# Kernel tuning notes

Hardware: AMD Instinct MI355X
Metric: run time of the kernel (lower is better)

The kernel has to match this reference:

```python
import jax, jax.numpy as jnp
import numpy as np

B, N, DEG = 16, 2048, 16          # graphs, nodes per graph, avg out-degree
C_IN, HID, K = 64, 128, 32        # in_channels, hidden_channels, out_channels (clusters)
NT = B * N                        # total nodes
E = NT * DEG                      # total edges
GN_EPS = 1e-5


def setup_inputs() -> dict:
    key = jax.random.key(0)
    ks = jax.random.split(key, 6)
    x = jax.random.normal(ks[0], (NT, C_IN), jnp.float32)
    # within-graph random edges (sorted batch => node i belongs to graph i // N)
    src_l = jax.random.randint(ks[1], (E,), 0, N)
    dst_l = jax.random.randint(ks[2], (E,), 0, N)
    gid = jnp.repeat(jnp.arange(B, dtype=jnp.int32), N * DEG)
    edge_index = jnp.stack([gid * N + src_l, gid * N + dst_l]).astype(jnp.int32)
    batch = jnp.repeat(jnp.arange(B, dtype=jnp.int32), N)
    return dict(
        x=x, edge_index=edge_index, batch=batch,
        gn_weight=jnp.ones((C_IN,), jnp.float32),
        gn_bias=jnp.zeros((C_IN,), jnp.float32),
        gn_mean_scale=jnp.ones((C_IN,), jnp.float32),
        w1=jax.random.normal(ks[3], (C_IN, HID), jnp.float32) / np.float32(np.sqrt(C_IN)),
        b1=jnp.zeros((HID,), jnp.float32),
        w2=jax.random.normal(ks[4], (HID, K), jnp.float32) / np.float32(np.sqrt(HID)),
        b2=jnp.zeros((K,), jnp.float32),
    )


def reference(x, gn_weight, gn_bias, gn_mean_scale, w1, b1, w2, b2, edge_index, batch):
    # ---- GraphNorm (per-graph mean/var with learnable mean scale) ----
    ones_n = jnp.ones((NT,), x.dtype)
    cnt = jax.ops.segment_sum(ones_n, batch, num_segments=B)[:, None]        # [B,1]
    mean = jax.ops.segment_sum(x, batch, num_segments=B) / cnt              # [B,C]
    xm = x - gn_mean_scale * mean[batch]
    var = jax.ops.segment_sum(xm * xm, batch, num_segments=B) / cnt         # [B,C]
    h = gn_weight * xm / jnp.sqrt(var + GN_EPS)[batch] + gn_bias            # [NT,C_IN]

    # ---- GCNConv (add self-loops, symmetric D^-1/2 (A+I) D^-1/2) ----
    src, dst = edge_index[0], edge_index[1]
    loop = jnp.arange(NT, dtype=src.dtype)
    src_l = jnp.concatenate([src, loop])
    dst_l = jnp.concatenate([dst, loop])
    deg = jax.ops.segment_sum(jnp.ones_like(src_l, x.dtype), dst_l, num_segments=NT)
    dinv = jnp.where(deg > 0, jax.lax.rsqrt(deg), 0.0)
    norm = dinv[src_l] * dinv[dst_l]                                        # [E+NT]
    hw = h @ w1                                                             # [NT,HID]
    h = jax.ops.segment_sum(norm[:, None] * hw[src_l], dst_l, num_segments=NT) + b1
    h = jax.nn.selu(h)

    # ---- to_dense_batch / to_dense_adj (uniform graph sizes -> mask all True) ----
    xd = h.reshape(B, N, HID)                                               # [B,N,F]
    adj = jnp.zeros((B, N, N), x.dtype).at[batch[src], src % N, dst % N].add(1.0)

    # ---- DMoNPooling ----
    s = jax.nn.softmax(xd @ w2 + b2, axis=-1)                               # [B,N,K]
    out = jax.nn.selu(jnp.einsum('bnk,bnf->bkf', s, xd))                    # [B,K,F]
    sta = jnp.einsum('bnk,bnm->bkm', s, adj)                                # [B,K,N]
    out_adj = jnp.einsum('bkm,bml->bkl', sta, s)                            # [B,K,K]

    degrees = adj.sum(-1)                                                   # [B,N]
    m = degrees.sum(-1) / 2                                                 # [B]
    ca = jnp.einsum('bnk,bn->bk', s, degrees)                               # [B,K]
    normalizer = ca[:, :, None] * ca[:, None, :] / 2 / m[:, None, None]
    spectral_loss = (-jnp.einsum('bkk->b', out_adj - normalizer) / (2 * m)).mean()

    ss = jnp.einsum('bnk,bnl->bkl', s, s)                                   # [B,K,K]
    ss_fro = jnp.sqrt(jnp.sum(ss * ss, axis=(-2, -1), keepdims=True))
    eye = jnp.eye(K, dtype=x.dtype)
    diff = ss / ss_fro - eye / jnp.sqrt(jnp.float32(K))
    ortho_loss = jnp.sqrt(jnp.sum(diff * diff, axis=(-2, -1))).mean()

    cluster_size = s.sum(1)                                                 # [B,K]
    cluster_loss = (jnp.linalg.norm(cluster_size, axis=1) / N
                    * jnp.sqrt(jnp.float32(K)) - 1).mean()
    # (coarsened-adj renormalization in DMoNPooling is unused by Net's outputs)

    return jax.nn.log_softmax(out, axis=-1), spectral_loss + ortho_loss + cluster_loss, s
```

## Files before the change

### kernel.cpp

```cpp
#include <hip/hip_runtime.h>
#include <cmath>

static constexpr int B_  = 16;
static constexpr int N_  = 2048;
static constexpr int NT_ = 32768;
static constexpr int E_  = 524288;

static constexpr size_t OFF_HSC    = 0;
static constexpr size_t OFF_XD     = 2097152;
static constexpr size_t OFF_SWS    = 6291456;
static constexpr size_t OFF_PART   = 7340032;
static constexpr size_t OFF_DINV   = 9437184;
static constexpr size_t OFF_GSP    = 9469952;
static constexpr size_t OFF_GSP2   = 9478144;
static constexpr size_t OFF_SSP    = 9486336;
static constexpr size_t OFF_CAP    = 10010624;
static constexpr size_t OFF_CSP    = 10027008;
static constexpr size_t OFF_SPECP  = 10043392;
static constexpr size_t OFF_ICNTO  = 10043904;
static constexpr size_t OFF_IROWS  = 10076672;
static constexpr size_t OFF_IESRC  = 10109444;

__device__ __forceinline__ float selu_f(float x) {
  return 1.0507009873554805f * (x > 0.f ? x : 1.6732632423543772f * expm1f(x));
}

__device__ __forceinline__ float block_sum_bcast(float v, float* sm) {
  int lane = threadIdx.x & 63, w = threadIdx.x >> 6;
#pragma unroll
  for (int off = 32; off; off >>= 1) v += __shfl_down(v, off);
  __syncthreads();
  if (lane == 0) sm[w] = v;
  __syncthreads();
  return sm[0] + sm[1] + sm[2] + sm[3];
}

__global__ __launch_bounds__(1024) void k_graph(const int* ei, const float* x,
                                                int* rows, int* esrc, int* cout_,
                                                float* dinv, float* gsp, float* gsp2) {
  __shared__ int hin[2048], hout[2048], sb[1024];
  __shared__ float l1[16][64], l2[16][64];
  int blk = blockIdx.x;
  int tid = threadIdx.x;
  if (blk < 16) {
    int g = blk;
    int nbase = g * 2048;
    int ebase = g * 32768;
    hin[tid] = 0; hin[tid + 1024] = 0;
    hout[tid] = 0; hout[tid + 1024] = 0;
    __syncthreads();
    for (int i = tid; i < 32768; i += 1024) {
      int s = ei[ebase + i];
      int d = ei[E_ + ebase + i];
      atomicAdd(&hout[s - nbase], 1);
      atomicAdd(&hin[d - nbase], 1);
    }
    __syncthreads();
    int a = hin[2 * tid], b2 = hin[2 * tid + 1];
    sb[tid] = a + b2;
    __syncthreads();
    for (int off = 1; off < 1024; off <<= 1) {
      int add = (tid >= off) ? sb[tid - off] : 0;
      __syncthreads();
      sb[tid] += add;
      __syncthreads();
    }
    int pref = (tid > 0) ? sb[tid - 1] : 0;
    int r0 = ebase + pref, r1 = r0 + a;
    int n0 = nbase + 2 * tid;
    rows[n0] = r0; rows[n0 + 1] = r1;
    dinv[n0] = rsqrtf((float)(a + 1));
    dinv[n0 + 1] = rsqrtf((float)(b2 + 1));
    cout_[n0] = hout[2 * tid];
    cout_[n0 + 1] = hout[2 * tid + 1];
    if (blk == 15 && tid == 1023) rows[NT_] = E_;
    __syncthreads();
    hin[2 * tid] = r0; hin[2 * tid + 1] = r1;
    __syncthreads();
    for (int i = tid; i < 32768; i += 1024) {
      int s = ei[ebase + i];
      int d = ei[E_ + ebase + i];
      int pos = atomicAdd(&hin[d - nbase], 1);
      esrc[pos] = s;
    }
  } else {
    int gi = blk - 16;
    int b = gi >> 3, chunk = gi & 7;
    int c = tid & 63, r = tid >> 6;
    float s = 0.f, s2 = 0.f;
    const float* xb = x + ((size_t)b * N_ + (size_t)chunk * 256) * 64;
    for (int n = r; n < 256; n += 16) {
      float v = xb[n * 64 + c];
      s += v; s2 += v * v;
    }
    l1[r][c] = s; l2[r][c] = s2;
    __syncthreads();
    if (r == 0) {
      float t1 = 0.f, t2 = 0.f;
#pragma unroll
      for (int i = 0; i < 16; i++) { t1 += l1[i][c]; t2 += l2[i][c]; }
      gsp[gi * 64 + c] = t1;
      gsp2[gi * 64 + c] = t2;
    }
  }
}

__global__ void k_prep(const float* x, const float* gsp, const float* gsp2,
                       const float* gw, const float* gb, const float* gms,
                       const float* dinv, float* hsc) {
  __shared__ float shs[64], scs[64];
  int tid = threadIdx.x;
  int bgr = blockIdx.x >> 7;
  if (tid < 64) {
    float s = 0.f, s2 = 0.f;
#pragma unroll
    for (int c8 = 0; c8 < 8; c8++) {
      s  += gsp[(bgr * 8 + c8) * 64 + tid];
      s2 += gsp2[(bgr * 8 + c8) * 64 + tid];
    }
    float mean = s * (1.f / 2048.f);
    float a = gms[tid];
    float var = s2 * (1.f / 2048.f) - (2.f * a - a * a) * mean * mean;
    shs[tid] = a * mean;
    scs[tid] = gw[tid] * rsqrtf(var + 1e-5f);
  }
  __syncthreads();
  int idx = blockIdx.x * 256 + tid;
  int node = idx >> 4, g4 = (idx & 15) * 4;
  float di = dinv[node];
  float4 xv = *(const float4*)&x[(size_t)node * 64 + g4];
  float4 bb = *(const float4*)&gb[g4];
  float4 o;
  o.x = ((xv.x - shs[g4])     * scs[g4]     + bb.x) * di;
  o.y = ((xv.y - shs[g4 + 1]) * scs[g4 + 1] + bb.y) * di;
  o.z = ((xv.z - shs[g4 + 2]) * scs[g4 + 2] + bb.z) * di;
  o.w = ((xv.w - shs[g4 + 3]) * scs[g4 + 3] + bb.w) * di;
  *(float4*)&hsc[(size_t)node * 64 + g4] = o;
}

__global__ __launch_bounds__(256) void k_mm1(const float* hsc, const float* dinv,
                                             const int* rows, const int* esrc,
                                             const float* w1, const float* b1,
                                             float* xd) {
  __shared__ float at[32 * 65];
  int tid = threadIdx.x;
  int n0 = blockIdx.x * 32;
  int wv = tid >> 6, c = tid & 63;
  for (int i = 0; i < 8; i++) {
    int nn = i * 4 + wv;
    int node = n0 + nn;
    int e0 = rows[node], e1 = rows[node + 1];
    float dd = dinv[node];
    float acc = hsc[(size_t)node * 64 + c];
    for (int e = e0; e < e1; e += 8) {
      int sidx[8]; float wt[8], hv[8];
#pragma unroll
      for (int j = 0; j < 8; j++) {
        int ee = e + j;
        sidx[j] = esrc[ee < e1 ? ee : e0];
        wt[j] = (ee < e1) ? 1.f : 0.f;
      }
#pragma unroll
      for (int j = 0; j < 8; j++) hv[j] = hsc[(size_t)sidx[j] * 64 + c];
#pragma unroll
      for (int j = 0; j < 8; j++) acc += wt[j] * hv[j];
    }
    at[nn * 65 + c] = dd * acc;
  }
  __syncthreads();
  int tx = tid & 31, ty = tid >> 5;
  int f0 = tx * 4, nn = ty * 4;
  float acc[4][4] = {};
  for (int k = 0; k < 64; k++) {
    float4 wvv = *(const float4*)&w1[k * 128 + f0];
#pragma unroll
    for (int i = 0; i < 4; i++) {
      float av = at[(nn + i) * 65 + k];
      acc[i][0] += av * wvv.x; acc[i][1] += av * wvv.y;
      acc[i][2] += av * wvv.z; acc[i][3] += av * wvv.w;
    }
  }
  float4 bv = *(const float4*)&b1[f0];
#pragma unroll
  for (int i = 0; i < 4; i++) {
    float4 o;
    o.x = selu_f(acc[i][0] + bv.x);
    o.y = selu_f(acc[i][1] + bv.y);
    o.z = selu_f(acc[i][2] + bv.z);
    o.w = selu_f(acc[i][3] + bv.w);
    *(float4*)&xd[(size_t)(n0 + nn + i) * 128 + f0] = o;
  }
}

__global__ __launch_bounds__(256) void k_mm2f(const float* xd, const float* w2,
                                              const float* b2, const int* cout_,
                                              float* s_ws, float* outs, float* ssp,
                                              float* cap, float* csp, float* part) {
  __shared__ float xt[64 * 129];
  __shared__ float w2s[128 * 32];
  __shared__ float st[64 * 33];
  __shared__ float r1[8][32], r2[8][32];
  int tid = threadIdx.x;
  int blk = blockIdx.x;
  int n0 = blk * 64;
  for (int i = tid; i < 4096; i += 256) w2s[i] = w2[i];
  for (int i = tid; i < 2048; i += 256) {
    int n = i >> 5, j4 = (i & 31) * 4;
    float4 v = *(const float4*)&xd[(size_t)(n0 + n) * 128 + j4];
    xt[n * 129 + j4] = v.x; xt[n * 129 + j4 + 1] = v.y;
    xt[n * 129 + j4 + 2] = v.z; xt[n * 129 + j4 + 3] = v.w;
  }
  __syncthreads();
  int ty = tid >> 3;
  int k0 = (tid & 7) * 4;
  float acc2[2][4] = {};
  for (int j = 0; j < 128; j++) {
    float4 wv = *(float4*)&w2s[j * 32 + k0];
    float x0 = xt[(ty * 2) * 129 + j];
    float x1 = xt[(ty * 2 + 1) * 129 + j];
    acc2[0][0] += x0 * wv.x; acc2[0][1] += x0 * wv.y; acc2[0][2] += x0 * wv.z; acc2[0][3] += x0 * wv.w;
    acc2[1][0] += x1 * wv.x; acc2[1][1] += x1 * wv.y; acc2[1][2] += x1 * wv.z; acc2[1][3] += x1 * wv.w;
  }
  float4 bv2 = *(const float4*)&b2[k0];
#pragma unroll
  for (int i = 0; i < 2; i++) {
    int n = ty * 2 + i;
    st[n * 33 + k0]     = acc2[i][0] + bv2.x;
    st[n * 33 + k0 + 1] = acc2[i][1] + bv2.y;
    st[n * 33 + k0 + 2] = acc2[i][2] + bv2.z;
    st[n * 33 + k0 + 3] = acc2[i][3] + bv2.w;
  }
  __syncthreads();
  if (tid < 64) {
    float m = -3.4e38f;
    for (int kk = 0; kk < 32; kk++) m = fmaxf(m, st[tid * 33 + kk]);
    float ssum = 0.f;
    for (int kk = 0; kk < 32; kk++) {
      float e = expf(st[tid * 33 + kk] - m);
      st[tid * 33 + kk] = e; ssum += e;
    }
    float inv = 1.f / ssum;
    for (int kk = 0; kk < 32; kk++) st[tid * 33 + kk] *= inv;
  }
  __syncthreads();
  for (int i = tid; i < 512; i += 256) {
    int n = i >> 3, q = (i & 7) * 4;
    float4 o = {st[n * 33 + q], st[n * 33 + q + 1], st[n * 33 + q + 2], st[n * 33 + q + 3]};
    *(float4*)&s_ws[(size_t)(n0 + n) * 32 + q] = o;
    float* op = &outs[(size_t)(n0 + n) * 32 + q];
    op[0] = o.x; op[1] = o.y; op[2] = o.z; op[3] = o.w;
  }
  {
    int k = tid >> 3, l0 = (tid & 7) * 4;
    float a0 = 0, a1 = 0, a2 = 0, a3 = 0;
    for (int n = 0; n < 64; n++) {
      float sk = st[n * 33 + k];
      a0 += sk * st[n * 33 + l0];     a1 += sk * st[n * 33 + l0 + 1];
      a2 += sk * st[n * 33 + l0 + 2]; a3 += sk * st[n * 33 + l0 + 3];
    }
    float4 o = {a0, a1, a2, a3};
    *(float4*)&ssp[(size_t)blk * 1024 + k * 32 + l0] = o;
  }
  {
    int k2 = tid & 31, r = tid >> 5;
    float aca = 0.f, acs = 0.f;
    for (int i = 0; i < 8; i++) {
      int n = i * 8 + r;
      float dg = (float)cout_[n0 + n];
      float v = st[n * 33 + k2];
      acs += v; aca += v * dg;
    }
    r1[r][k2] = aca; r2[r][k2] = acs;
    __syncthreads();
    if (r == 0) {
      float sa = 0.f, sc = 0.f;
#pragma unroll
      for (int i = 0; i < 8; i++) { sa += r1[i][k2]; sc += r2[i][k2]; }
      cap[blk * 32 + k2] = sa;
      csp[blk * 32 + k2] = sc;
    }
  }
  {
    int tx = tid & 31, ty2 = tid >> 5;
    int f0 = tx * 4, kk0 = ty2 * 4;
    float acc[4][4] = {};
    for (int n = 0; n < 64; n++) {
      float s0 = st[n * 33 + kk0], s1 = st[n * 33 + kk0 + 1];
      float s2 = st[n * 33 + kk0 + 2], s3 = st[n * 33 + kk0 + 3];
      float4 xv = {xt[n * 129 + f0], xt[n * 129 + f0 + 1], xt[n * 129 + f0 + 2], xt[n * 129 + f0 + 3]};
      acc[0][0] += s0 * xv.x; acc[0][1] += s0 * xv.y; acc[0][2] += s0 * xv.z; acc[0][3] += s0 * xv.w;
      acc[1][0] += s1 * xv.x; acc[1][1] += s1 * xv.y; acc[1][2] += s1 * xv.z; acc[1][3] += s1 * xv.w;
      acc[2][0] += s2 * xv.x; acc[2][1] += s2 * xv.y; acc[2][2] += s2 * xv.z; acc[2][3] += s2 * xv.w;
      acc[3][0] += s3 * xv.x; acc[3][1] += s3 * xv.y; acc[3][2] += s3 * xv.z; acc[3][3] += s3 * xv.w;
    }
#pragma unroll
    for (int i = 0; i < 4; i++) {
      float4 o = {acc[i][0], acc[i][1], acc[i][2], acc[i][3]};
      *(float4*)&part[(size_t)(blk * 32 + kk0 + i) * 128 + f0] = o;
    }
  }
}

__global__ __launch_bounds__(256) void k_spec(const int* ei, const float* s_ws,
                                              float* specp, float* lossp) {
  __shared__ float sm4[4];
  int blk = blockIdx.x, tid = threadIdx.x;
  if (blk == 0 && tid == 0) lossp[0] = 0.f;
  int ebase = blk * 1024;
  float acc = 0.f;
#pragma unroll
  for (int j = 0; j < 4; j++) {
    int e = ebase + j * 256 + tid;
    int s = ei[e], d = ei[E_ + e];
    const float4* ap = (const float4*)&s_ws[(size_t)s * 32];
    const float4* cp = (const float4*)&s_ws[(size_t)d * 32];
#pragma unroll
    for (int q = 0; q < 8; q++) {
      float4 u = ap[q], v = cp[q];
      acc += u.x * v.x + u.y * v.y + u.z * v.z + u.w * v.w;
    }
  }
  int lane = tid & 63, w = tid >> 6;
#pragma unroll
  for (int off = 32; off; off >>= 1) acc += __shfl_down(acc, off);
  if (lane == 0) sm4[w] = acc;
  __syncthreads();
  if (tid == 0) specp[blk] = sm4[0] + sm4[1] + sm4[2] + sm4[3];
}

__global__ void k_outf(const float* part, float* out0) {
  int row = blockIdx.x;
  int b = row >> 5, k = row & 31;
  int f = threadIdx.x;
  float v = 0.f;
#pragma unroll
  for (int c = 0; c < 32; c++) v += part[(size_t)((b * 32 + c) * 32 + k) * 128 + f];
  v = selu_f(v);
  int lane = threadIdx.x & 63, w = threadIdx.x >> 6;
  __shared__ float s1[2], s2[2];
  float m = v;
#pragma unroll
  for (int off = 32; off; off >>= 1) m = fmaxf(m, __shfl_down(m, off));
  if (lane == 0) s1[w] = m;
  __syncthreads();
  m = fmaxf(s1[0], s1[1]);
  float e = expf(v - m), t = e;
#pragma unroll
  for (int off = 32; off; off >>= 1) t += __shfl_down(t, off);
  if (lane == 0) s2[w] = t;
  __syncthreads();
  float tot = s2[0] + s2[1];
  out0[(size_t)row * 128 + f] = v - m - logf(tot);
}

__global__ void k_loss(const float* ssp, const float* csp, const float* cap,
                       const float* specp, float* loss) {
  int b = blockIdx.x;
  __shared__ float sm[4];
  int tid = threadIdx.x;
  float v0 = 0, v1 = 0, v2 = 0, v3 = 0;
  for (int c = 0; c < 32; c++) {
    float4 u = *(const float4*)&ssp[(size_t)(b * 32 + c) * 1024 + tid * 4];
    v0 += u.x; v1 += u.y; v2 += u.z; v3 += u.w;
  }
  float ssq = v0 * v0 + v1 * v1 + v2 * v2 + v3 * v3;
  ssq = block_sum_bcast(ssq, sm);
  float inv = 1.f / sqrtf(ssq);
  float dsq = 0.f;
  {
    int i0 = tid * 4;
    float vv[4] = {v0, v1, v2, v3};
#pragma unroll
    for (int j = 0; j < 4; j++) {
      int i = i0 + j;
      float d = vv[j] * inv;
      if ((i >> 5) == (i & 31)) d -= 0.17677669529663687f;
      dsq += d * d;
    }
  }
  dsq = block_sum_bcast(dsq, sm);
  float csq = 0.f, casq = 0.f;
  if (tid < 32) {
    float c1 = 0.f, c2 = 0.f;
    for (int c = 0; c < 32; c++) {
      c1 += csp[(size_t)(b * 32 + c) * 32 + tid];
      c2 += cap[(size_t)(b * 32 + c) * 32 + tid];
    }
    csq = c1 * c1; casq = c2 * c2;
  }
  csq = block_sum_bcast(csq, sm);
  casq = block_sum_bcast(casq, sm);
  float spec_sum = (tid < 32) ? specp[b * 32 + tid] : 0.f;
  spec_sum = block_sum_bcast(spec_sum, sm);
  if (tid == 0) {
    float ortho = sqrtf(dsq);
    float cl = sqrtf(csq) * (1.f / 2048.f) * 5.656854249492381f - 1.f;
    float m = 16384.f;
    float spec = -(spec_sum - casq / (2.f * m)) / (2.f * m);
    atomicAdd(loss, (spec + ortho + cl) * (1.f / 16.f));
  }
}

extern "C" void kernel_launch(void* const* d_in, const int* in_sizes, int n_in,
                              void* d_out, int out_size, void* d_ws, size_t ws_size,
                              hipStream_t stream) {
  (void)in_sizes; (void)n_in; (void)out_size; (void)ws_size;
  const float* x   = (const float*)d_in[0];
  const int*   ei  = (const int*)d_in[1];
  const float* gw  = (const float*)d_in[3];
  const float* gb  = (const float*)d_in[4];
  const float* gms = (const float*)d_in[5];
  const float* w1  = (const float*)d_in[6];
  const float* b1  = (const float*)d_in[7];
  const float* w2  = (const float*)d_in[8];
  const float* b2  = (const float*)d_in[9];
  float* out = (float*)d_out;
  float* ws  = (float*)d_ws;

  float* hsc    = ws + OFF_HSC;
  float* xd     = ws + OFF_XD;
  float* s_ws   = ws + OFF_SWS;
  float* part   = ws + OFF_PART;
  float* dinv   = ws + OFF_DINV;
  float* gsp    = ws + OFF_GSP;
  float* gsp2   = ws + OFF_GSP2;
  float* ssp    = ws + OFF_SSP;
  float* cap    = ws + OFF_CAP;
  float* csp    = ws + OFF_CSP;
  float* specp  = ws + OFF_SPECP;
  int*   cout_  = (int*)(ws + OFF_ICNTO);
  int*   rows   = (int*)(ws + OFF_IROWS);
  int*   esrc   = (int*)(ws + OFF_IESRC);

  float* out0  = out;
  float* lossp = out + 65536;
  float* outs  = out + 65537;

  hipLaunchKernelGGL(k_graph, dim3(144), dim3(1024), 0, stream,
                     ei, x, rows, esrc, cout_, dinv, gsp, gsp2);
  hipLaunchKernelGGL(k_prep, dim3(2048), dim3(256), 0, stream,
                     x, gsp, gsp2, gw, gb, gms, dinv, hsc);
  hipLaunchKernelGGL(k_mm1, dim3(1024), dim3(256), 0, stream, hsc, dinv, rows, esrc, w1, b1, xd);
  hipLaunchKernelGGL(k_mm2f, dim3(512), dim3(256), 0, stream,
                     xd, w2, b2, cout_, s_ws, outs, ssp, cap, csp, part);
  hipLaunchKernelGGL(k_spec, dim3(512), dim3(256), 0, stream, ei, s_ws, specp, lossp);
  hipLaunchKernelGGL(k_outf, dim3(512), dim3(128), 0, stream, part, out0);
  hipLaunchKernelGGL(k_loss, dim3(16), dim3(256), 0, stream, ssp, csp, cap, specp, lossp);
}
```

Baseline: 207.9 us.

## Split CSR build into parallel count, scan, and global-atomic scatter phases

The single per-graph kernel that counted degrees, scanned and scattered edges on only 16 blocks is split up. Counting now runs on 128 blocks with shared histograms merged by global atomics, a separate 16-block kernel does the prefix scan and dinv, and the edge scatter moves into k_prep using global atomic cursors. This spreads the serial CSR build over many more CUs at the cost of an extra memset, an extra launch, and contended global atomics. Within each destination node the esrc order becomes nondeterministic.

```diff
diff --git a/kernel.cpp b/kernel.cpp
--- a/kernel.cpp
+++ b/kernel.cpp
@@ -17,9 +17,11 @@
 static constexpr size_t OFF_CAP    = 10010624;
 static constexpr size_t OFF_CSP    = 10027008;
 static constexpr size_t OFF_SPECP  = 10043392;
-static constexpr size_t OFF_ICNTO  = 10043904;
-static constexpr size_t OFF_IROWS  = 10076672;
-static constexpr size_t OFF_IESRC  = 10109444;
+static constexpr size_t OFF_ICNTI  = 10043904;
+static constexpr size_t OFF_ICNTO  = 10076672;
+static constexpr size_t OFF_IROWS  = 10109440;
+static constexpr size_t OFF_ICURS  = 10142212;
+static constexpr size_t OFF_IESRC  = 10174980;
 
 __device__ __forceinline__ float selu_f(float x) {
   return 1.0507009873554805f * (x > 0.f ? x : 1.6732632423543772f * expm1f(x));
@@ -35,56 +37,33 @@
   return sm[0] + sm[1] + sm[2] + sm[3];
 }
 
-__global__ __launch_bounds__(1024) void k_graph(const int* ei, const float* x,
-                                                int* rows, int* esrc, int* cout_,
-                                                float* dinv, float* gsp, float* gsp2) {
-  __shared__ int hin[2048], hout[2048], sb[1024];
+__global__ __launch_bounds__(1024) void k_count(const int* ei, const float* x,
+                                                int* cin, int* cout_,
+                                                float* gsp, float* gsp2) {
+  __shared__ int hin[2048], hout[2048];
   __shared__ float l1[16][64], l2[16][64];
   int blk = blockIdx.x;
   int tid = threadIdx.x;
-  if (blk < 16) {
-    int g = blk;
-    int nbase = g * 2048;
-    int ebase = g * 32768;
+  if (blk < 128) {
+    int g = blk >> 3, j = blk & 7;
+    int nbase = g * 2048, ebase = g * 32768 + j * 4096;
     hin[tid] = 0; hin[tid + 1024] = 0;
     hout[tid] = 0; hout[tid + 1024] = 0;
     __syncthreads();
-    for (int i = tid; i < 32768; i += 1024) {
-      int s = ei[ebase + i];
-      int d = ei[E_ + ebase + i];
+#pragma unroll
+    for (int it = 0; it < 4; it++) {
+      int e = ebase + it * 1024 + tid;
+      int s = ei[e], d = ei[E_ + e];
       atomicAdd(&hout[s - nbase], 1);
       atomicAdd(&hin[d - nbase], 1);
     }
     __syncthreads();
-    int a = hin[2 * tid], b2 = hin[2 * tid + 1];
-    sb[tid] = a + b2;
-    __syncthreads();
-    for (int off = 1; off < 1024; off <<= 1) {
-      int add = (tid >= off) ? sb[tid - off] : 0;
-      __syncthreads();
-      sb[tid] += add;
-      __syncthreads();
-    }
-    int pref = (tid > 0) ? sb[tid - 1] : 0;
-    int r0 = ebase + pref, r1 = r0 + a;
-    int n0 = nbase + 2 * tid;
-    rows[n0] = r0; rows[n0 + 1] = r1;
-    dinv[n0] = rsqrtf((float)(a + 1));
-    dinv[n0 + 1] = rsqrtf((float)(b2 + 1));
-    cout_[n0] = hout[2 * tid];
-    cout_[n0 + 1] = hout[2 * tid + 1];
-    if (blk == 15 && tid == 1023) rows[NT_] = E_;
-    __syncthreads();
-    hin[2 * tid] = r0; hin[2 * tid + 1] = r1;
-    __syncthreads();
-    for (int i = tid; i < 32768; i += 1024) {
-      int s = ei[ebase + i];
-      int d = ei[E_ + ebase + i];
-      int pos = atomicAdd(&hin[d - nbase], 1);
-      esrc[pos] = s;
-    }
+    atomicAdd(&cin[nbase + tid], hin[tid]);
+    atomicAdd(&cin[nbase + tid + 1024], hin[tid + 1024]);
+    atomicAdd(&cout_[nbase + tid], hout[tid]);
+    atomicAdd(&cout_[nbase + tid + 1024], hout[tid + 1024]);
   } else {
-    int gi = blk - 16;
+    int gi = blk - 128;
     int b = gi >> 3, chunk = gi & 7;
     int c = tid & 63, r = tid >> 6;
     float s = 0.f, s2 = 0.f;
@@ -105,9 +84,34 @@
   }
 }
 
+__global__ __launch_bounds__(1024) void k_scan(const int* cin, int* rows, int* curs,
+                                               float* dinv) {
+  __shared__ int sb[1024];
+  int g = blockIdx.x, tid = threadIdx.x;
+  int nbase = g * 2048, ebase = g * 32768;
+  int a = cin[nbase + 2 * tid], b2 = cin[nbase + 2 * tid + 1];
+  sb[tid] = a + b2;
+  __syncthreads();
+  for (int off = 1; off < 1024; off <<= 1) {
+    int add = (tid >= off) ? sb[tid - off] : 0;
+    __syncthreads();
+    sb[tid] += add;
+    __syncthreads();
+  }
+  int pref = (tid > 0) ? sb[tid - 1] : 0;
+  int r0 = ebase + pref, r1 = r0 + a;
+  int n0 = nbase + 2 * tid;
+  rows[n0] = r0; rows[n0 + 1] = r1;
+  curs[n0] = r0; curs[n0 + 1] = r1;
+  dinv[n0] = rsqrtf((float)(a + 1));
+  dinv[n0 + 1] = rsqrtf((float)(b2 + 1));
+  if (g == 15 && tid == 1023) rows[NT_] = E_;
+}
+
 __global__ void k_prep(const float* x, const float* gsp, const float* gsp2,
                        const float* gw, const float* gb, const float* gms,
-                       const float* dinv, float* hsc) {
+                       const float* dinv, float* hsc,
+                       const int* ei, int* curs, int* esrc) {
   __shared__ float shs[64], scs[64];
   int tid = threadIdx.x;
   int bgr = blockIdx.x >> 7;
@@ -136,6 +140,9 @@
   o.z = ((xv.z - shs[g4 + 2]) * scs[g4 + 2] + bb.z) * di;
   o.w = ((xv.w - shs[g4 + 3]) * scs[g4 + 3] + bb.w) * di;
   *(float4*)&hsc[(size_t)node * 64 + g4] = o;
+  int s = ei[idx], d = ei[E_ + idx];
+  int pos = atomicAdd(&curs[d], 1);
+  esrc[pos] = s;
 }
 
 __global__ __launch_bounds__(256) void k_mm1(const float* hsc, const float* dinv,
@@ -428,18 +435,21 @@
   float* cap    = ws + OFF_CAP;
   float* csp    = ws + OFF_CSP;
   float* specp  = ws + OFF_SPECP;
+  int*   cin    = (int*)(ws + OFF_ICNTI);
   int*   cout_  = (int*)(ws + OFF_ICNTO);
   int*   rows   = (int*)(ws + OFF_IROWS);
+  int*   curs   = (int*)(ws + OFF_ICURS);
   int*   esrc   = (int*)(ws + OFF_IESRC);
 
   float* out0  = out;
   float* lossp = out + 65536;
   float* outs  = out + 65537;
 
-  hipLaunchKernelGGL(k_graph, dim3(144), dim3(1024), 0, stream,
-                     ei, x, rows, esrc, cout_, dinv, gsp, gsp2);
+  hipMemsetAsync((void*)cin, 0, 2 * NT_ * sizeof(int), stream);
+  hipLaunchKernelGGL(k_count, dim3(256), dim3(1024), 0, stream, ei, x, cin, cout_, gsp, gsp2);
+  hipLaunchKernelGGL(k_scan, dim3(16), dim3(1024), 0, stream, cin, rows, curs, dinv);
   hipLaunchKernelGGL(k_prep, dim3(2048), dim3(256), 0, stream,
-                     x, gsp, gsp2, gw, gb, gms, dinv, hsc);
+                     x, gsp, gsp2, gw, gb, gms, dinv, hsc, ei, curs, esrc);
   hipLaunchKernelGGL(k_mm1, dim3(1024), dim3(256), 0, stream, hsc, dinv, rows, esrc, w1, b1, xd);
   hipLaunchKernelGGL(k_mm2f, dim3(512), dim3(256), 0, stream,
                      xd, w2, b2, cout_, s_ws, outs, ssp, cap, csp, part);
```

Measured after the change: 208.0 us. Within noise of the previous version (+0.1%).
